# Kernel tuning notes

Measured on AMD Instinct MI355X. Metric: run time of the kernel, lower is better.

## Reference

```python
import jax, jax.numpy as jnp
import numpy as np

NUM_HEADS = 4
WINDOW = 64  # 8*8


def setup_inputs() -> dict:
    key = jax.random.key(0)
    ks = jax.random.split(key, 8)
    C = 128
    x = jax.random.normal(ks[0], (16, C, 128, 128), dtype=jnp.float32)
    s = 0.02
    Wq = jax.random.normal(ks[1], (C, C), dtype=jnp.float32) * s
    bq = jax.random.normal(ks[2], (C,), dtype=jnp.float32) * s
    Wk = jax.random.normal(ks[3], (C, C), dtype=jnp.float32) * s
    bk = jax.random.normal(ks[4], (C,), dtype=jnp.float32) * s
    Wv = jax.random.normal(ks[5], (C, C), dtype=jnp.float32) * s
    bv = jax.random.normal(ks[6], (C,), dtype=jnp.float32) * s
    Bbias = jnp.zeros((WINDOW, WINDOW), dtype=jnp.float32)
    return {"x": x, "Wq": Wq, "bq": bq, "Wk": Wk, "bk": bk, "Wv": Wv, "bv": bv, "Bbias": Bbias}


def reference(x, Wq, bq, Wk, bk, Wv, bv, Bbias):
    B, C, H, W = x.shape
    nW = (H * W) // WINDOW
    h = NUM_HEADS
    d = C // h
    # (B,C,H,W) -> (B,H,W,C) -> (B, nW, WINDOW, C)
    xr = jnp.transpose(x, (0, 2, 3, 1)).reshape(B, nW, WINDOW, C)
    # torch Linear: y = x @ W.T + b
    q = xr @ Wq.T + bq
    k = xr @ Wk.T + bk
    v = xr @ Wv.T + bv
    # split heads: (B, nW, WINDOW, h, d) -> (B, nW, h, WINDOW, d)
    def split(t):
        return jnp.transpose(t.reshape(B, nW, WINDOW, h, d), (0, 1, 3, 2, 4))
    Q, K, V = split(q), split(k), split(v)
    scale = 1.0 / jnp.sqrt(jnp.asarray(d, dtype=x.dtype))
    scores = jnp.einsum('bnhqd,bnhkd->bnhqk', Q, K) * scale + Bbias
    probs = jax.nn.softmax(scores, axis=-1)
    out = jnp.einsum('bnhqk,bnhkd->bnhqd', probs, V)
    # (B, nW, h, WINDOW, d) -> (B, nW, WINDOW, C) -> (B,H,W,C) -> (B,C,H,W)
    out = jnp.transpose(out, (0, 1, 3, 2, 4)).reshape(B, H, W, C)
    return jnp.transpose(out, (0, 3, 1, 2))
```

## Files before the change

kernel.cpp:

```cpp
#include <hip/hip_runtime.h>
#include <hip/hip_bf16.h>


typedef __attribute__((ext_vector_type(8))) short bf16x8;
typedef __attribute__((ext_vector_type(4))) float f32x4;

__device__ __forceinline__ ushort f2bf(float f) {
    __hip_bfloat16 h = __float2bfloat16(f);
    ushort u; __builtin_memcpy(&u, &h, 2); return u;
}
__device__ __forceinline__ unsigned pk2(float a, float b) {
    __hip_bfloat162 h = __float22bfloat162_rn(make_float2(a, b));
    unsigned u; __builtin_memcpy(&u, &h, 4); return u;
}
__device__ __forceinline__ int fsw(int row) { return ((row ^ (row >> 4)) & 15) << 4; }

__global__ void wconv(const float* __restrict__ Wq, const float* __restrict__ Wk,
                      const float* __restrict__ Wv, ushort* __restrict__ out) {
    int i = blockIdx.x * 256 + threadIdx.x;
    out[i]         = f2bf(Wq[i]);
    out[16384 + i] = f2bf(Wk[i]);
    out[32768 + i] = f2bf(Wv[i]);
}

__global__ __launch_bounds__(256, 2)
void attn_win(const float* __restrict__ x, const ushort* __restrict__ wbf,
              const float* __restrict__ bq, const float* __restrict__ bk,
              const float* __restrict__ bv, const float* __restrict__ Bb,
              float* __restrict__ out) {
    __shared__ __align__(16) char sX[16384];

    const int tid = threadIdx.x;
    const int w = tid >> 6;
    const int l = tid & 63;
    const int lr = l & 15;
    const int lg = (l >> 4) & 3;
    const int blk = blockIdx.x;
    const int b = blk >> 8, n = blk & 255;
    const long xbase = (long)b * 128 * 16384 + n * 64;

    const int s0 = 32 * (lg & 1) + lr;
    const int s1 = s0 + 16;
    const bool hi2 = (lg >> 1);

    #pragma unroll
    for (int it = 0; it < 2; ++it) {
        int idx = it * 256 + tid;
        int cq = idx >> 4, t4 = idx & 15;
        const float* px = x + xbase + (long)(4 * cq) * 16384 + t4 * 4;
        float4 v0 = *(const float4*)(px);
        float4 v1 = *(const float4*)(px + 16384);
        float4 v2 = *(const float4*)(px + 32768);
        float4 v3 = *(const float4*)(px + 49152);
        float a0[4] = {v0.x, v0.y, v0.z, v0.w};
        float a1[4] = {v1.x, v1.y, v1.z, v1.w};
        float a2[4] = {v2.x, v2.y, v2.z, v2.w};
        float a3[4] = {v3.x, v3.y, v3.z, v3.w};
        #pragma unroll
        for (int jj = 0; jj < 4; ++jj) {
            int t = t4 * 4 + jj;
            uint2 pk;
            pk.x = pk2(a0[jj], a1[jj]);
            pk.y = pk2(a2[jj], a3[jj]);
            *(uint2*)(sX + t * 256 + ((8 * cq) ^ fsw(t))) = pk;
        }
    }
    __syncthreads();

    bf16x8 fQ[4], fK[4];
    {
        f32x4 accQ[2][4], accK[2][4];
        #pragma unroll
        for (int tn = 0; tn < 2; ++tn) {
            float4 bbq = *(const float4*)(bq + 32 * w + 16 * tn + 4 * lg);
            float4 bbk = *(const float4*)(bk + 32 * w + 16 * tn + 4 * lg);
            #pragma unroll
            for (int tm = 0; tm < 4; ++tm) {
                accQ[tn][tm] = (f32x4){bbq.x, bbq.y, bbq.z, bbq.w};
                accK[tn][tm] = (f32x4){bbk.x, bbk.y, bbk.z, bbk.w};
            }
        }
        #pragma unroll
        for (int kk = 0; kk < 4; ++kk) {
            bf16x8 aXk[4];
            #pragma unroll
            for (int tm = 0; tm < 4; ++tm) {
                int row = 16 * tm + lr;
                aXk[tm] = *(const bf16x8*)(sX + row * 256
                              + (((8 * lg + 32 * kk) * 2) ^ fsw(row)));
            }
            bf16x8 bWq[2], bWk[2];
            #pragma unroll
            for (int tn = 0; tn < 2; ++tn) {
                int orow = (32 * w + 16 * tn + lr) * 128 + 8 * lg + 32 * kk;
                bWq[tn] = *(const bf16x8*)(wbf + orow);
                bWk[tn] = *(const bf16x8*)(wbf + 16384 + orow);
            }
            #pragma unroll
            for (int tn = 0; tn < 2; ++tn)
                #pragma unroll
                for (int tm = 0; tm < 4; ++tm) {
                    accQ[tn][tm] = __builtin_amdgcn_mfma_f32_16x16x32_bf16(
                        bWq[tn], aXk[tm], accQ[tn][tm], 0, 0, 0);
                    accK[tn][tm] = __builtin_amdgcn_mfma_f32_16x16x32_bf16(
                        bWk[tn], aXk[tm], accK[tn][tm], 0, 0, 0);
                }
        }
        #pragma unroll
        for (int p = 0; p < 2; ++p) {
            unsigned qpk[4][2][2];
            #pragma unroll
            for (int tm = 0; tm < 4; ++tm)
                #pragma unroll
                for (int tn = 0; tn < 2; ++tn) {
                    const f32x4& a = (p == 0) ? accQ[tn][tm] : accK[tn][tm];
                    qpk[tm][tn][0] = pk2(a[0], a[1]);
                    qpk[tm][tn][1] = pk2(a[2], a[3]);
                }
            #pragma unroll
            for (int tm = 0; tm < 4; ++tm) {
                int t00 = __shfl((int)qpk[tm][0][0], s0);
                int t01 = __shfl((int)qpk[tm][0][1], s0);
                int t10 = __shfl((int)qpk[tm][1][0], s0);
                int t11 = __shfl((int)qpk[tm][1][1], s0);
                int u00 = __shfl((int)qpk[tm][0][0], s1);
                int u01 = __shfl((int)qpk[tm][0][1], s1);
                int u10 = __shfl((int)qpk[tm][1][0], s1);
                int u11 = __shfl((int)qpk[tm][1][1], s1);
                int4 wv;
                wv.x = hi2 ? t10 : t00;
                wv.y = hi2 ? t11 : t01;
                wv.z = hi2 ? u10 : u00;
                wv.w = hi2 ? u11 : u01;
                if (p == 0) fQ[tm] = *(bf16x8*)&wv;
                else        fK[tm] = *(bf16x8*)&wv;
            }
        }
    }

    bf16x8 fV[2][2];
    {
        const ushort* wp = wbf + 32768;
        f32x4 acc[4][2];
        #pragma unroll
        for (int tn = 0; tn < 2; ++tn) {
            float bias = bv[32 * w + 16 * tn + lr];
            #pragma unroll
            for (int tmi = 0; tmi < 4; ++tmi)
                acc[tmi][tn] = (f32x4){bias, bias, bias, bias};
        }
        #pragma unroll
        for (int kk = 0; kk < 4; ++kk) {
            bf16x8 aXk[4];
            #pragma unroll
            for (int tmi = 0; tmi < 4; ++tmi) {
                int row = 16 * tmi + lr;
                aXk[tmi] = *(const bf16x8*)(sX + row * 256
                               + (((8 * lg + 32 * kk) * 2) ^ fsw(row)));
            }
            bf16x8 bW[2];
            #pragma unroll
            for (int tn = 0; tn < 2; ++tn)
                bW[tn] = *(const bf16x8*)(wp + (32 * w + 16 * tn + lr) * 128 + 8 * lg + 32 * kk);
            #pragma unroll
            for (int tmi = 0; tmi < 4; ++tmi)
                #pragma unroll
                for (int tn = 0; tn < 2; ++tn)
                    acc[tmi][tn] = __builtin_amdgcn_mfma_f32_16x16x32_bf16(
                        aXk[tmi], bW[tn], acc[tmi][tn], 0, 0, 0);
        }
        unsigned vpk[4][2][2];
        #pragma unroll
        for (int tmi = 0; tmi < 4; ++tmi)
            #pragma unroll
            for (int tn = 0; tn < 2; ++tn) {
                vpk[tmi][tn][0] = pk2(acc[tmi][tn][0], acc[tmi][tn][1]);
                vpk[tmi][tn][1] = pk2(acc[tmi][tn][2], acc[tmi][tn][3]);
            }
        #pragma unroll
        for (int kk2 = 0; kk2 < 2; ++kk2)
            #pragma unroll
            for (int tn = 0; tn < 2; ++tn) {
                int tmA = 2 * kk2, tmB = 2 * kk2 + 1;
                int a0 = __shfl((int)vpk[tmA][tn][0], s0);
                int a1 = __shfl((int)vpk[tmA][tn][1], s0);
                int a2 = __shfl((int)vpk[tmA][tn][0], s1);
                int a3 = __shfl((int)vpk[tmA][tn][1], s1);
                int b0 = __shfl((int)vpk[tmB][tn][0], s0);
                int b1 = __shfl((int)vpk[tmB][tn][1], s0);
                int b2 = __shfl((int)vpk[tmB][tn][0], s1);
                int b3 = __shfl((int)vpk[tmB][tn][1], s1);
                int4 wv;
                wv.x = hi2 ? b0 : a0;
                wv.y = hi2 ? b1 : a1;
                wv.z = hi2 ? b2 : a2;
                wv.w = hi2 ? b3 : a3;
                fV[kk2][tn] = *(bf16x8*)&wv;
            }
    }

    f32x4 sc[4][4];
    #pragma unroll
    for (int tmK = 0; tmK < 4; ++tmK)
        #pragma unroll
        for (int tmQ = 0; tmQ < 4; ++tmQ) {
            sc[tmK][tmQ] = (f32x4){0.f, 0.f, 0.f, 0.f};
            sc[tmK][tmQ] = __builtin_amdgcn_mfma_f32_16x16x32_bf16(
                fK[tmK], fQ[tmQ], sc[tmK][tmQ], 0, 0, 0);
        }

    const float scale = 0.17677669529663687f;
    const float L2E = 1.4426950408889634f;
    #pragma unroll
    for (int tmQ = 0; tmQ < 4; ++tmQ) {
        int q = 16 * tmQ + lr;
        float s = 0.f;
        #pragma unroll
        for (int tmK = 0; tmK < 4; ++tmK) {
            float4 bb = *(const float4*)(Bb + q * 64 + 16 * tmK + 4 * lg);
            float e0 = exp2f((sc[tmK][tmQ][0] * scale + bb.x) * L2E);
            float e1 = exp2f((sc[tmK][tmQ][1] * scale + bb.y) * L2E);
            float e2 = exp2f((sc[tmK][tmQ][2] * scale + bb.z) * L2E);
            float e3 = exp2f((sc[tmK][tmQ][3] * scale + bb.w) * L2E);
            sc[tmK][tmQ][0] = e0; sc[tmK][tmQ][1] = e1;
            sc[tmK][tmQ][2] = e2; sc[tmK][tmQ][3] = e3;
            s += (e0 + e1) + (e2 + e3);
        }
        s += __shfl_xor(s, 16);
        s += __shfl_xor(s, 32);
        float rs = 1.0f / s;
        #pragma unroll
        for (int tmK = 0; tmK < 4; ++tmK)
            #pragma unroll
            for (int r = 0; r < 4; ++r)
                sc[tmK][tmQ][r] *= rs;
    }

    unsigned pks[4][4][2];
    #pragma unroll
    for (int tmK = 0; tmK < 4; ++tmK)
        #pragma unroll
        for (int tmQ = 0; tmQ < 4; ++tmQ) {
            pks[tmK][tmQ][0] = pk2(sc[tmK][tmQ][0], sc[tmK][tmQ][1]);
            pks[tmK][tmQ][1] = pk2(sc[tmK][tmQ][2], sc[tmK][tmQ][3]);
        }

    f32x4 o[4][2];
    #pragma unroll
    for (int tmq = 0; tmq < 4; ++tmq)
        #pragma unroll
        for (int tn = 0; tn < 2; ++tn)
            o[tmq][tn] = (f32x4){0.f, 0.f, 0.f, 0.f};
    #pragma unroll
    for (int kk2 = 0; kk2 < 2; ++kk2) {
        int tmA = 2 * kk2, tmB = 2 * kk2 + 1;
        #pragma unroll
        for (int tmq = 0; tmq < 4; ++tmq) {
            int a0 = __shfl((int)pks[tmA][tmq][0], s0);
            int b0 = __shfl((int)pks[tmB][tmq][0], s0);
            int a1 = __shfl((int)pks[tmA][tmq][1], s0);
            int b1 = __shfl((int)pks[tmB][tmq][1], s0);
            int a2 = __shfl((int)pks[tmA][tmq][0], s1);
            int b2 = __shfl((int)pks[tmB][tmq][0], s1);
            int a3 = __shfl((int)pks[tmA][tmq][1], s1);
            int b3 = __shfl((int)pks[tmB][tmq][1], s1);
            int4 wv;
            wv.x = hi2 ? b0 : a0;
            wv.y = hi2 ? b1 : a1;
            wv.z = hi2 ? b2 : a2;
            wv.w = hi2 ? b3 : a3;
            bf16x8 aP = *(bf16x8*)&wv;
            #pragma unroll
            for (int tn = 0; tn < 2; ++tn)
                o[tmq][tn] = __builtin_amdgcn_mfma_f32_16x16x32_bf16(
                    aP, fV[kk2][tn], o[tmq][tn], 0, 0, 0);
        }
    }

    #pragma unroll
    for (int tmq = 0; tmq < 4; ++tmq)
        #pragma unroll
        for (int tn = 0; tn < 2; ++tn) {
            int ch = 32 * w + 16 * tn + lr;
            int tok = 16 * tmq + 4 * lg;
            float4 ov;
            ov.x = o[tmq][tn][0];
            ov.y = o[tmq][tn][1];
            ov.z = o[tmq][tn][2];
            ov.w = o[tmq][tn][3];
            *(float4*)(out + xbase + (long)ch * 16384 + tok) = ov;
        }
}

extern "C" void kernel_launch(void* const* d_in, const int* in_sizes, int n_in,
                              void* d_out, int out_size, void* d_ws, size_t ws_size,
                              hipStream_t stream) {
    const float* x  = (const float*)d_in[0];
    const float* Wq = (const float*)d_in[1];
    const float* bq = (const float*)d_in[2];
    const float* Wk = (const float*)d_in[3];
    const float* bk = (const float*)d_in[4];
    const float* Wv = (const float*)d_in[5];
    const float* bv = (const float*)d_in[6];
    const float* Bb = (const float*)d_in[7];
    float* out = (float*)d_out;
    ushort* wbf = (ushort*)d_ws;

    wconv<<<64, 256, 0, stream>>>(Wq, Wk, Wv, wbf);
    attn_win<<<4096, 256, 0, stream>>>(x, wbf, bq, bk, bv, Bb, out);
}
```

Measured before the change: 114.3 us.

## Process two windows per block with all global loads issued up front

Each block now handles two adjacent 64-token windows, so the grid is halved. Every x load for both windows is issued before any conversion, which puts more memory requests in flight per thread. The two windows are then computed one after another from separate LDS buffers. Shared memory doubles to 32KB and register pressure during the load phase rises, which may cut occupancy. Compute for the second window does not overlap with loads for a later block.

After: 199.8 us. 1.75x slower.

```diff
diff --git a/kernel.cpp b/kernel.cpp
--- a/kernel.cpp
+++ b/kernel.cpp
@@ -28,7 +28,7 @@
               const float* __restrict__ bq, const float* __restrict__ bk,
               const float* __restrict__ bv, const float* __restrict__ Bb,
               float* __restrict__ out) {
-    __shared__ __align__(16) char sX[16384];
+    __shared__ __align__(16) char sX[2][16384];
 
     const int tid = threadIdx.x;
     const int w = tid >> 6;
@@ -36,260 +36,278 @@
     const int lr = l & 15;
     const int lg = (l >> 4) & 3;
     const int blk = blockIdx.x;
-    const int b = blk >> 8, n = blk & 255;
-    const long xbase = (long)b * 128 * 16384 + n * 64;
+    const int gw0 = 2 * blk;
+    const long xbase0 = (long)(gw0 >> 8) * 128 * 16384 + (long)(gw0 & 255) * 64;
 
     const int s0 = 32 * (lg & 1) + lr;
     const int s1 = s0 + 16;
     const bool hi2 = (lg >> 1);
 
-    #pragma unroll
-    for (int it = 0; it < 2; ++it) {
-        int idx = it * 256 + tid;
-        int cq = idx >> 4, t4 = idx & 15;
-        const float* px = x + xbase + (long)(4 * cq) * 16384 + t4 * 4;
-        float4 v0 = *(const float4*)(px);
-        float4 v1 = *(const float4*)(px + 16384);
-        float4 v2 = *(const float4*)(px + 32768);
-        float4 v3 = *(const float4*)(px + 49152);
-        float a0[4] = {v0.x, v0.y, v0.z, v0.w};
-        float a1[4] = {v1.x, v1.y, v1.z, v1.w};
-        float a2[4] = {v2.x, v2.y, v2.z, v2.w};
-        float a3[4] = {v3.x, v3.y, v3.z, v3.w};
-        #pragma unroll
-        for (int jj = 0; jj < 4; ++jj) {
-            int t = t4 * 4 + jj;
-            uint2 pk;
-            pk.x = pk2(a0[jj], a1[jj]);
-            pk.y = pk2(a2[jj], a3[jj]);
-            *(uint2*)(sX + t * 256 + ((8 * cq) ^ fsw(t))) = pk;
-        }
+    {
+        float4 pf[2][2][4];
+        #pragma unroll
+        for (int wi = 0; wi < 2; ++wi)
+            #pragma unroll
+            for (int it = 0; it < 2; ++it) {
+                int idx = it * 256 + tid;
+                int cq = idx >> 4, t4 = idx & 15;
+                const float* px = x + xbase0 + wi * 64 + (long)(4 * cq) * 16384 + t4 * 4;
+                pf[wi][it][0] = *(const float4*)(px);
+                pf[wi][it][1] = *(const float4*)(px + 16384);
+                pf[wi][it][2] = *(const float4*)(px + 32768);
+                pf[wi][it][3] = *(const float4*)(px + 49152);
+            }
+        #pragma unroll
+        for (int wi = 0; wi < 2; ++wi)
+            #pragma unroll
+            for (int it = 0; it < 2; ++it) {
+                int idx = it * 256 + tid;
+                int cq = idx >> 4, t4 = idx & 15;
+                float a0[4] = {pf[wi][it][0].x, pf[wi][it][0].y, pf[wi][it][0].z, pf[wi][it][0].w};
+                float a1[4] = {pf[wi][it][1].x, pf[wi][it][1].y, pf[wi][it][1].z, pf[wi][it][1].w};
+                float a2[4] = {pf[wi][it][2].x, pf[wi][it][2].y, pf[wi][it][2].z, pf[wi][it][2].w};
+                float a3[4] = {pf[wi][it][3].x, pf[wi][it][3].y, pf[wi][it][3].z, pf[wi][it][3].w};
+                #pragma unroll
+                for (int jj = 0; jj < 4; ++jj) {
+                    int t = t4 * 4 + jj;
+                    uint2 pk;
+                    pk.x = pk2(a0[jj], a1[jj]);
+                    pk.y = pk2(a2[jj], a3[jj]);
+                    *(uint2*)(&sX[wi][0] + t * 256 + ((8 * cq) ^ fsw(t))) = pk;
+                }
+            }
     }
     __syncthreads();
 
-    bf16x8 fQ[4], fK[4];
-    {
-        f32x4 accQ[2][4], accK[2][4];
-        #pragma unroll
-        for (int tn = 0; tn < 2; ++tn) {
-            float4 bbq = *(const float4*)(bq + 32 * w + 16 * tn + 4 * lg);
-            float4 bbk = *(const float4*)(bk + 32 * w + 16 * tn + 4 * lg);
-            #pragma unroll
-            for (int tm = 0; tm < 4; ++tm) {
-                accQ[tn][tm] = (f32x4){bbq.x, bbq.y, bbq.z, bbq.w};
-                accK[tn][tm] = (f32x4){bbk.x, bbk.y, bbk.z, bbk.w};
+    #pragma unroll 1
+    for (int wi = 0; wi < 2; ++wi) {
+        const char* sXw = &sX[wi][0];
+        const long xb = xbase0 + wi * 64;
+
+        bf16x8 fQ[4], fK[4];
+        {
+            f32x4 accQ[2][4], accK[2][4];
+            #pragma unroll
+            for (int tn = 0; tn < 2; ++tn) {
+                float4 bbq = *(const float4*)(bq + 32 * w + 16 * tn + 4 * lg);
+                float4 bbk = *(const float4*)(bk + 32 * w + 16 * tn + 4 * lg);
+                #pragma unroll
+                for (int tm = 0; tm < 4; ++tm) {
+                    accQ[tn][tm] = (f32x4){bbq.x, bbq.y, bbq.z, bbq.w};
+                    accK[tn][tm] = (f32x4){bbk.x, bbk.y, bbk.z, bbk.w};
+                }
+            }
+            #pragma unroll
+            for (int kk = 0; kk < 4; ++kk) {
+                bf16x8 aXk[4];
+                #pragma unroll
+                for (int tm = 0; tm < 4; ++tm) {
+                    int row = 16 * tm + lr;
+                    aXk[tm] = *(const bf16x8*)(sXw + row * 256
+                                  + (((8 * lg + 32 * kk) * 2) ^ fsw(row)));
+                }
+                bf16x8 bWq[2], bWk[2];
+                #pragma unroll
+                for (int tn = 0; tn < 2; ++tn) {
+                    int orow = (32 * w + 16 * tn + lr) * 128 + 8 * lg + 32 * kk;
+                    bWq[tn] = *(const bf16x8*)(wbf + orow);
+                    bWk[tn] = *(const bf16x8*)(wbf + 16384 + orow);
+                }
+                #pragma unroll
+                for (int tn = 0; tn < 2; ++tn)
+                    #pragma unroll
+                    for (int tm = 0; tm < 4; ++tm) {
+                        accQ[tn][tm] = __builtin_amdgcn_mfma_f32_16x16x32_bf16(
+                            bWq[tn], aXk[tm], accQ[tn][tm], 0, 0, 0);
+                        accK[tn][tm] = __builtin_amdgcn_mfma_f32_16x16x32_bf16(
+                            bWk[tn], aXk[tm], accK[tn][tm], 0, 0, 0);
+                    }
+            }
+            #pragma unroll
+            for (int p = 0; p < 2; ++p) {
+                unsigned qpk[4][2][2];
+                #pragma unroll
+                for (int tm = 0; tm < 4; ++tm)
+                    #pragma unroll
+                    for (int tn = 0; tn < 2; ++tn) {
+                        const f32x4& a = (p == 0) ? accQ[tn][tm] : accK[tn][tm];
+                        qpk[tm][tn][0] = pk2(a[0], a[1]);
+                        qpk[tm][tn][1] = pk2(a[2], a[3]);
+                    }
+                #pragma unroll
+                for (int tm = 0; tm < 4; ++tm) {
+                    int t00 = __shfl((int)qpk[tm][0][0], s0);
+                    int t01 = __shfl((int)qpk[tm][0][1], s0);
+                    int t10 = __shfl((int)qpk[tm][1][0], s0);
+                    int t11 = __shfl((int)qpk[tm][1][1], s0);
+                    int u00 = __shfl((int)qpk[tm][0][0], s1);
+                    int u01 = __shfl((int)qpk[tm][0][1], s1);
+                    int u10 = __shfl((int)qpk[tm][1][0], s1);
+                    int u11 = __shfl((int)qpk[tm][1][1], s1);
+                    int4 wv;
+                    wv.x = hi2 ? t10 : t00;
+                    wv.y = hi2 ? t11 : t01;
+                    wv.z = hi2 ? u10 : u00;
+                    wv.w = hi2 ? u11 : u01;
+                    if (p == 0) fQ[tm] = *(bf16x8*)&wv;
+                    else        fK[tm] = *(bf16x8*)&wv;
+                }
             }
         }
-        #pragma unroll
-        for (int kk = 0; kk < 4; ++kk) {
-            bf16x8 aXk[4];
-            #pragma unroll
-            for (int tm = 0; tm < 4; ++tm) {
-                int row = 16 * tm + lr;
-                aXk[tm] = *(const bf16x8*)(sX + row * 256
-                              + (((8 * lg + 32 * kk) * 2) ^ fsw(row)));
-            }
-            bf16x8 bWq[2], bWk[2];
+
+        bf16x8 fV[2][2];
+        {
+            const ushort* wp = wbf + 32768;
+            f32x4 acc[4][2];
             #pragma unroll
             for (int tn = 0; tn < 2; ++tn) {
-                int orow = (32 * w + 16 * tn + lr) * 128 + 8 * lg + 32 * kk;
-                bWq[tn] = *(const bf16x8*)(wbf + orow);
-                bWk[tn] = *(const bf16x8*)(wbf + 16384 + orow);
-            }
+                float bias = bv[32 * w + 16 * tn + lr];
+                #pragma unroll
+                for (int tmi = 0; tmi < 4; ++tmi)
+                    acc[tmi][tn] = (f32x4){bias, bias, bias, bias};
+            }
+            #pragma unroll
+            for (int kk = 0; kk < 4; ++kk) {
+                bf16x8 aXk[4];
+                #pragma unroll
+                for (int tmi = 0; tmi < 4; ++tmi) {
+                    int row = 16 * tmi + lr;
+                    aXk[tmi] = *(const bf16x8*)(sXw + row * 256
+                                   + (((8 * lg + 32 * kk) * 2) ^ fsw(row)));
+                }
+                bf16x8 bW[2];
+                #pragma unroll
+                for (int tn = 0; tn < 2; ++tn)
+                    bW[tn] = *(const bf16x8*)(wp + (32 * w + 16 * tn + lr) * 128 + 8 * lg + 32 * kk);
+                #pragma unroll
+                for (int tmi = 0; tmi < 4; ++tmi)
+                    #pragma unroll
+                    for (int tn = 0; tn < 2; ++tn)
+                        acc[tmi][tn] = __builtin_amdgcn_mfma_f32_16x16x32_bf16(
+                            aXk[tmi], bW[tn], acc[tmi][tn], 0, 0, 0);
+            }
+            unsigned vpk[4][2][2];
+            #pragma unroll
+            for (int tmi = 0; tmi < 4; ++tmi)
+                #pragma unroll
+                for (int tn = 0; tn < 2; ++tn) {
+                    vpk[tmi][tn][0] = pk2(acc[tmi][tn][0], acc[tmi][tn][1]);
+                    vpk[tmi][tn][1] = pk2(acc[tmi][tn][2], acc[tmi][tn][3]);
+                }
+            #pragma unroll
+            for (int kk2 = 0; kk2 < 2; ++kk2)
+                #pragma unroll
+                for (int tn = 0; tn < 2; ++tn) {
+                    int tmA = 2 * kk2, tmB = 2 * kk2 + 1;
+                    int a0 = __shfl((int)vpk[tmA][tn][0], s0);
+                    int a1 = __shfl((int)vpk[tmA][tn][1], s0);
+                    int a2 = __shfl((int)vpk[tmA][tn][0], s1);
+                    int a3 = __shfl((int)vpk[tmA][tn][1], s1);
+                    int b0 = __shfl((int)vpk[tmB][tn][0], s0);
+                    int b1 = __shfl((int)vpk[tmB][tn][1], s0);
+                    int b2 = __shfl((int)vpk[tmB][tn][0], s1);
+                    int b3 = __shfl((int)vpk[tmB][tn][1], s1);
+                    int4 wv;
+                    wv.x = hi2 ? b0 : a0;
+                    wv.y = hi2 ? b1 : a1;
+                    wv.z = hi2 ? b2 : a2;
+                    wv.w = hi2 ? b3 : a3;
+                    fV[kk2][tn] = *(bf16x8*)&wv;
+                }
+        }
+
+        f32x4 sc[4][4];
+        #pragma unroll
+        for (int tmK = 0; tmK < 4; ++tmK)
+            #pragma unroll
+            for (int tmQ = 0; tmQ < 4; ++tmQ) {
+                sc[tmK][tmQ] = (f32x4){0.f, 0.f, 0.f, 0.f};
+                sc[tmK][tmQ] = __builtin_amdgcn_mfma_f32_16x16x32_bf16(
+                    fK[tmK], fQ[tmQ], sc[tmK][tmQ], 0, 0, 0);
+            }
+
+        const float scale = 0.17677669529663687f;
+        const float L2E = 1.4426950408889634f;
+        #pragma unroll
+        for (int tmQ = 0; tmQ < 4; ++tmQ) {
+            int q = 16 * tmQ + lr;
+            float s = 0.f;
+            #pragma unroll
+            for (int tmK = 0; tmK < 4; ++tmK) {
+                float4 bb = *(const float4*)(Bb + q * 64 + 16 * tmK + 4 * lg);
+                float e0 = exp2f((sc[tmK][tmQ][0] * scale + bb.x) * L2E);
+                float e1 = exp2f((sc[tmK][tmQ][1] * scale + bb.y) * L2E);
+                float e2 = exp2f((sc[tmK][tmQ][2] * scale + bb.z) * L2E);
+                float e3 = exp2f((sc[tmK][tmQ][3] * scale + bb.w) * L2E);
+                sc[tmK][tmQ][0] = e0; sc[tmK][tmQ][1] = e1;
+                sc[tmK][tmQ][2] = e2; sc[tmK][tmQ][3] = e3;
+                s += (e0 + e1) + (e2 + e3);
+            }
+            s += __shfl_xor(s, 16);
+            s += __shfl_xor(s, 32);
+            float rs = 1.0f / s;
+            #pragma unroll
+            for (int tmK = 0; tmK < 4; ++tmK)
+                #pragma unroll
+                for (int r = 0; r < 4; ++r)
+                    sc[tmK][tmQ][r] *= rs;
+        }
+
+        unsigned pks[4][4][2];
+        #pragma unroll
+        for (int tmK = 0; tmK < 4; ++tmK)
+            #pragma unroll
+            for (int tmQ = 0; tmQ < 4; ++tmQ) {
+                pks[tmK][tmQ][0] = pk2(sc[tmK][tmQ][0], sc[tmK][tmQ][1]);
+                pks[tmK][tmQ][1] = pk2(sc[tmK][tmQ][2], sc[tmK][tmQ][3]);
+            }
+
+        f32x4 o[4][2];
+        #pragma unroll
+        for (int tmq = 0; tmq < 4; ++tmq)
             #pragma unroll
             for (int tn = 0; tn < 2; ++tn)
-                #pragma unroll
-                for (int tm = 0; tm < 4; ++tm) {
-                    accQ[tn][tm] = __builtin_amdgcn_mfma_f32_16x16x32_bf16(
-                        bWq[tn], aXk[tm], accQ[tn][tm], 0, 0, 0);
-                    accK[tn][tm] = __builtin_amdgcn_mfma_f32_16x16x32_bf16(
-                        bWk[tn], aXk[tm], accK[tn][tm], 0, 0, 0);
-                }
-        }
-        #pragma unroll
-        for (int p = 0; p < 2; ++p) {
-            unsigned qpk[4][2][2];
-            #pragma unroll
-            for (int tm = 0; tm < 4; ++tm)
-                #pragma unroll
-                for (int tn = 0; tn < 2; ++tn) {
-                    const f32x4& a = (p == 0) ? accQ[tn][tm] : accK[tn][tm];
-                    qpk[tm][tn][0] = pk2(a[0], a[1]);
-                    qpk[tm][tn][1] = pk2(a[2], a[3]);
-                }
-            #pragma unroll
-            for (int tm = 0; tm < 4; ++tm) {
-                int t00 = __shfl((int)qpk[tm][0][0], s0);
-                int t01 = __shfl((int)qpk[tm][0][1], s0);
-                int t10 = __shfl((int)qpk[tm][1][0], s0);
-                int t11 = __shfl((int)qpk[tm][1][1], s0);
-                int u00 = __shfl((int)qpk[tm][0][0], s1);
-                int u01 = __shfl((int)qpk[tm][0][1], s1);
-                int u10 = __shfl((int)qpk[tm][1][0], s1);
-                int u11 = __shfl((int)qpk[tm][1][1], s1);
-                int4 wv;
-                wv.x = hi2 ? t10 : t00;
-                wv.y = hi2 ? t11 : t01;
-                wv.z = hi2 ? u10 : u00;
-                wv.w = hi2 ? u11 : u01;
-                if (p == 0) fQ[tm] = *(bf16x8*)&wv;
-                else        fK[tm] = *(bf16x8*)&wv;
-            }
-        }
-    }
-
-    bf16x8 fV[2][2];
-    {
-        const ushort* wp = wbf + 32768;
-        f32x4 acc[4][2];
-        #pragma unroll
-        for (int tn = 0; tn < 2; ++tn) {
-            float bias = bv[32 * w + 16 * tn + lr];
-            #pragma unroll
-            for (int tmi = 0; tmi < 4; ++tmi)
-                acc[tmi][tn] = (f32x4){bias, bias, bias, bias};
-        }
-        #pragma unroll
-        for (int kk = 0; kk < 4; ++kk) {
-            bf16x8 aXk[4];
-            #pragma unroll
-            for (int tmi = 0; tmi < 4; ++tmi) {
-                int row = 16 * tmi + lr;
-                aXk[tmi] = *(const bf16x8*)(sX + row * 256
-                               + (((8 * lg + 32 * kk) * 2) ^ fsw(row)));
-            }
-            bf16x8 bW[2];
-            #pragma unroll
-            for (int tn = 0; tn < 2; ++tn)
-                bW[tn] = *(const bf16x8*)(wp + (32 * w + 16 * tn + lr) * 128 + 8 * lg + 32 * kk);
-            #pragma unroll
-            for (int tmi = 0; tmi < 4; ++tmi)
-                #pragma unroll
-                for (int tn = 0; tn < 2; ++tn)
-                    acc[tmi][tn] = __builtin_amdgcn_mfma_f32_16x16x32_bf16(
-                        aXk[tmi], bW[tn], acc[tmi][tn], 0, 0, 0);
-        }
-        unsigned vpk[4][2][2];
-        #pragma unroll
-        for (int tmi = 0; tmi < 4; ++tmi)
-            #pragma unroll
-            for (int tn = 0; tn < 2; ++tn) {
-                vpk[tmi][tn][0] = pk2(acc[tmi][tn][0], acc[tmi][tn][1]);
-                vpk[tmi][tn][1] = pk2(acc[tmi][tn][2], acc[tmi][tn][3]);
-            }
-        #pragma unroll
-        for (int kk2 = 0; kk2 < 2; ++kk2)
-            #pragma unroll
-            for (int tn = 0; tn < 2; ++tn) {
-                int tmA = 2 * kk2, tmB = 2 * kk2 + 1;
-                int a0 = __shfl((int)vpk[tmA][tn][0], s0);
-                int a1 = __shfl((int)vpk[tmA][tn][1], s0);
-                int a2 = __shfl((int)vpk[tmA][tn][0], s1);
-                int a3 = __shfl((int)vpk[tmA][tn][1], s1);
-                int b0 = __shfl((int)vpk[tmB][tn][0], s0);
-                int b1 = __shfl((int)vpk[tmB][tn][1], s0);
-                int b2 = __shfl((int)vpk[tmB][tn][0], s1);
-                int b3 = __shfl((int)vpk[tmB][tn][1], s1);
+                o[tmq][tn] = (f32x4){0.f, 0.f, 0.f, 0.f};
+        #pragma unroll
+        for (int kk2 = 0; kk2 < 2; ++kk2) {
+            int tmA = 2 * kk2, tmB = 2 * kk2 + 1;
+            #pragma unroll
+            for (int tmq = 0; tmq < 4; ++tmq) {
+                int a0 = __shfl((int)pks[tmA][tmq][0], s0);
+                int b0 = __shfl((int)pks[tmB][tmq][0], s0);
+                int a1 = __shfl((int)pks[tmA][tmq][1], s0);
+                int b1 = __shfl((int)pks[tmB][tmq][1], s0);
+                int a2 = __shfl((int)pks[tmA][tmq][0], s1);
+                int b2 = __shfl((int)pks[tmB][tmq][0], s1);
+                int a3 = __shfl((int)pks[tmA][tmq][1], s1);
+                int b3 = __shfl((int)pks[tmB][tmq][1], s1);
                 int4 wv;
                 wv.x = hi2 ? b0 : a0;
                 wv.y = hi2 ? b1 : a1;
                 wv.z = hi2 ? b2 : a2;
                 wv.w = hi2 ? b3 : a3;
-                fV[kk2][tn] = *(bf16x8*)&wv;
+                bf16x8 aP = *(bf16x8*)&wv;
+                #pragma unroll
+                for (int tn = 0; tn < 2; ++tn)
+                    o[tmq][tn] = __builtin_amdgcn_mfma_f32_16x16x32_bf16(
+                        aP, fV[kk2][tn], o[tmq][tn], 0, 0, 0);
+            }
+        }
+
+        #pragma unroll
+        for (int tmq = 0; tmq < 4; ++tmq)
+            #pragma unroll
+            for (int tn = 0; tn < 2; ++tn) {
+                int ch = 32 * w + 16 * tn + lr;
+                int tok = 16 * tmq + 4 * lg;
+                float4 ov;
+                ov.x = o[tmq][tn][0];
+                ov.y = o[tmq][tn][1];
+                ov.z = o[tmq][tn][2];
+                ov.w = o[tmq][tn][3];
+                *(float4*)(out + xb + (long)ch * 16384 + tok) = ov;
             }
     }
-
-    f32x4 sc[4][4];
-    #pragma unroll
-    for (int tmK = 0; tmK < 4; ++tmK)
-        #pragma unroll
-        for (int tmQ = 0; tmQ < 4; ++tmQ) {
-            sc[tmK][tmQ] = (f32x4){0.f, 0.f, 0.f, 0.f};
-            sc[tmK][tmQ] = __builtin_amdgcn_mfma_f32_16x16x32_bf16(
-                fK[tmK], fQ[tmQ], sc[tmK][tmQ], 0, 0, 0);
-        }
-
-    const float scale = 0.17677669529663687f;
-    const float L2E = 1.4426950408889634f;
-    #pragma unroll
-    for (int tmQ = 0; tmQ < 4; ++tmQ) {
-        int q = 16 * tmQ + lr;
-        float s = 0.f;
-        #pragma unroll
-        for (int tmK = 0; tmK < 4; ++tmK) {
-            float4 bb = *(const float4*)(Bb + q * 64 + 16 * tmK + 4 * lg);
-            float e0 = exp2f((sc[tmK][tmQ][0] * scale + bb.x) * L2E);
-            float e1 = exp2f((sc[tmK][tmQ][1] * scale + bb.y) * L2E);
-            float e2 = exp2f((sc[tmK][tmQ][2] * scale + bb.z) * L2E);
-            float e3 = exp2f((sc[tmK][tmQ][3] * scale + bb.w) * L2E);
-            sc[tmK][tmQ][0] = e0; sc[tmK][tmQ][1] = e1;
-            sc[tmK][tmQ][2] = e2; sc[tmK][tmQ][3] = e3;
-            s += (e0 + e1) + (e2 + e3);
-        }
-        s += __shfl_xor(s, 16);
-        s += __shfl_xor(s, 32);
-        float rs = 1.0f / s;
-        #pragma unroll
-        for (int tmK = 0; tmK < 4; ++tmK)
-            #pragma unroll
-            for (int r = 0; r < 4; ++r)
-                sc[tmK][tmQ][r] *= rs;
-    }
-
-    unsigned pks[4][4][2];
-    #pragma unroll
-    for (int tmK = 0; tmK < 4; ++tmK)
-        #pragma unroll
-        for (int tmQ = 0; tmQ < 4; ++tmQ) {
-            pks[tmK][tmQ][0] = pk2(sc[tmK][tmQ][0], sc[tmK][tmQ][1]);
-            pks[tmK][tmQ][1] = pk2(sc[tmK][tmQ][2], sc[tmK][tmQ][3]);
-        }
-
-    f32x4 o[4][2];
-    #pragma unroll
-    for (int tmq = 0; tmq < 4; ++tmq)
-        #pragma unroll
-        for (int tn = 0; tn < 2; ++tn)
-            o[tmq][tn] = (f32x4){0.f, 0.f, 0.f, 0.f};
-    #pragma unroll
-    for (int kk2 = 0; kk2 < 2; ++kk2) {
-        int tmA = 2 * kk2, tmB = 2 * kk2 + 1;
-        #pragma unroll
-        for (int tmq = 0; tmq < 4; ++tmq) {
-            int a0 = __shfl((int)pks[tmA][tmq][0], s0);
-            int b0 = __shfl((int)pks[tmB][tmq][0], s0);
-            int a1 = __shfl((int)pks[tmA][tmq][1], s0);
-            int b1 = __shfl((int)pks[tmB][tmq][1], s0);
-            int a2 = __shfl((int)pks[tmA][tmq][0], s1);
-            int b2 = __shfl((int)pks[tmB][tmq][0], s1);
-            int a3 = __shfl((int)pks[tmA][tmq][1], s1);
-            int b3 = __shfl((int)pks[tmB][tmq][1], s1);
-            int4 wv;
-            wv.x = hi2 ? b0 : a0;
-            wv.y = hi2 ? b1 : a1;
-            wv.z = hi2 ? b2 : a2;
-            wv.w = hi2 ? b3 : a3;
-            bf16x8 aP = *(bf16x8*)&wv;
-            #pragma unroll
-            for (int tn = 0; tn < 2; ++tn)
-                o[tmq][tn] = __builtin_amdgcn_mfma_f32_16x16x32_bf16(
-                    aP, fV[kk2][tn], o[tmq][tn], 0, 0, 0);
-        }
-    }
-
-    #pragma unroll
-    for (int tmq = 0; tmq < 4; ++tmq)
-        #pragma unroll
-        for (int tn = 0; tn < 2; ++tn) {
-            int ch = 32 * w + 16 * tn + lr;
-            int tok = 16 * tmq + 4 * lg;
-            float4 ov;
-            ov.x = o[tmq][tn][0];
-            ov.y = o[tmq][tn][1];
-            ov.z = o[tmq][tn][2];
-            ov.w = o[tmq][tn][3];
-            *(float4*)(out + xbase + (long)ch * 16384 + tok) = ov;
-        }
 }
 
 extern "C" void kernel_launch(void* const* d_in, const int* in_sizes, int n_in,
@@ -307,5 +325,5 @@
     ushort* wbf = (ushort*)d_ws;
 
     wconv<<<64, 256, 0, stream>>>(Wq, Wk, Wv, wbf);
-    attn_win<<<4096, 256, 0, stream>>>(x, wbf, bq, bk, bv, Bb, out);
-}
+    attn_win<<<2048, 256, 0, stream>>>(x, wbf, bq, bk, bv, Bb, out);
+}
```

## Switch to 16x16x16 bf16 MFMA so accumulators feed next GEMM without shuffles

Applied to the files above, without the earlier changes.

Replaces the 16x16x32 bf16 MFMA with the 16x16x16 variant throughout the QKV projection, QK^T and PV stages. With K=16, the accumulator layout of one MFMA matches the operand layout the next one needs, so the cross-lane __shfl permutations that rebuilt Q, K, V and P fragments are dropped and results are packed to bf16 in place. The cost is twice as many MFMA instructions, each covering half the K depth, plus narrower 8-byte LDS and global loads. Score computation is also moved inside the per-query-tile softmax loop, which shortens register live ranges.

New measurement: 162.5 us. +42.2%, slower.

```diff
diff --git a/kernel.cpp b/kernel.cpp
--- a/kernel.cpp
+++ b/kernel.cpp
@@ -2,8 +2,10 @@
 #include <hip/hip_bf16.h>
 
 
-typedef __attribute__((ext_vector_type(8))) short bf16x8;
+typedef __attribute__((ext_vector_type(4))) short bf16x4;
 typedef __attribute__((ext_vector_type(4))) float f32x4;
+
+#define MFMA16(A, B, C) __builtin_amdgcn_mfma_f32_16x16x16bf16_1k((A), (B), (C), 0, 0, 0)
 
 __device__ __forceinline__ ushort f2bf(float f) {
     __hip_bfloat16 h = __float2bfloat16(f);
@@ -12,6 +14,10 @@
 __device__ __forceinline__ unsigned pk2(float a, float b) {
     __hip_bfloat162 h = __float22bfloat162_rn(make_float2(a, b));
     unsigned u; __builtin_memcpy(&u, &h, 4); return u;
+}
+__device__ __forceinline__ bf16x4 pk4(float a, float b, float c, float d) {
+    uint2 u; u.x = pk2(a, b); u.y = pk2(c, d);
+    bf16x4 r; __builtin_memcpy(&r, &u, 8); return r;
 }
 __device__ __forceinline__ int fsw(int row) { return ((row ^ (row >> 4)) & 15) << 4; }
 
@@ -38,10 +44,6 @@
     const int blk = blockIdx.x;
     const int b = blk >> 8, n = blk & 255;
     const long xbase = (long)b * 128 * 16384 + n * 64;
-
-    const int s0 = 32 * (lg & 1) + lr;
-    const int s1 = s0 + 16;
-    const bool hi2 = (lg >> 1);
 
     #pragma unroll
     for (int it = 0; it < 2; ++it) {
@@ -67,163 +69,113 @@
     }
     __syncthreads();
 
-    bf16x8 fQ[4], fK[4];
-    {
-        f32x4 accQ[2][4], accK[2][4];
-        #pragma unroll
-        for (int tn = 0; tn < 2; ++tn) {
-            float4 bbq = *(const float4*)(bq + 32 * w + 16 * tn + 4 * lg);
-            float4 bbk = *(const float4*)(bk + 32 * w + 16 * tn + 4 * lg);
+    f32x4 accQ[2][4], accK[2][4];
+    #pragma unroll
+    for (int tn = 0; tn < 2; ++tn) {
+        float4 bbq = *(const float4*)(bq + 32 * w + 16 * tn + 4 * lg);
+        float4 bbk = *(const float4*)(bk + 32 * w + 16 * tn + 4 * lg);
+        #pragma unroll
+        for (int tm = 0; tm < 4; ++tm) {
+            accQ[tn][tm] = (f32x4){bbq.x, bbq.y, bbq.z, bbq.w};
+            accK[tn][tm] = (f32x4){bbk.x, bbk.y, bbk.z, bbk.w};
+        }
+    }
+    #pragma unroll
+    for (int kk = 0; kk < 8; ++kk) {
+        bf16x4 aXk[4];
+        #pragma unroll
+        for (int tm = 0; tm < 4; ++tm) {
+            int row = 16 * tm + lr;
+            aXk[tm] = *(const bf16x4*)(sX + row * 256
+                          + ((32 * kk + 8 * lg) ^ fsw(row)));
+        }
+        bf16x4 wq[2], wk[2];
+        #pragma unroll
+        for (int tn = 0; tn < 2; ++tn) {
+            int off = (32 * w + 16 * tn + lr) * 128 + 16 * kk + 4 * lg;
+            wq[tn] = *(const bf16x4*)(wbf + off);
+            wk[tn] = *(const bf16x4*)(wbf + 16384 + off);
+        }
+        #pragma unroll
+        for (int tn = 0; tn < 2; ++tn)
             #pragma unroll
             for (int tm = 0; tm < 4; ++tm) {
-                accQ[tn][tm] = (f32x4){bbq.x, bbq.y, bbq.z, bbq.w};
-                accK[tn][tm] = (f32x4){bbk.x, bbk.y, bbk.z, bbk.w};
+                accQ[tn][tm] = MFMA16(wq[tn], aXk[tm], accQ[tn][tm]);
+                accK[tn][tm] = MFMA16(wk[tn], aXk[tm], accK[tn][tm]);
             }
-        }
-        #pragma unroll
-        for (int kk = 0; kk < 4; ++kk) {
-            bf16x8 aXk[4];
-            #pragma unroll
-            for (int tm = 0; tm < 4; ++tm) {
-                int row = 16 * tm + lr;
-                aXk[tm] = *(const bf16x8*)(sX + row * 256
-                              + (((8 * lg + 32 * kk) * 2) ^ fsw(row)));
-            }
-            bf16x8 bWq[2], bWk[2];
-            #pragma unroll
-            for (int tn = 0; tn < 2; ++tn) {
-                int orow = (32 * w + 16 * tn + lr) * 128 + 8 * lg + 32 * kk;
-                bWq[tn] = *(const bf16x8*)(wbf + orow);
-                bWk[tn] = *(const bf16x8*)(wbf + 16384 + orow);
-            }
-            #pragma unroll
-            for (int tn = 0; tn < 2; ++tn)
-                #pragma unroll
-                for (int tm = 0; tm < 4; ++tm) {
-                    accQ[tn][tm] = __builtin_amdgcn_mfma_f32_16x16x32_bf16(
-                        bWq[tn], aXk[tm], accQ[tn][tm], 0, 0, 0);
-                    accK[tn][tm] = __builtin_amdgcn_mfma_f32_16x16x32_bf16(
-                        bWk[tn], aXk[tm], accK[tn][tm], 0, 0, 0);
-                }
-        }
-        #pragma unroll
-        for (int p = 0; p < 2; ++p) {
-            unsigned qpk[4][2][2];
-            #pragma unroll
-            for (int tm = 0; tm < 4; ++tm)
-                #pragma unroll
-                for (int tn = 0; tn < 2; ++tn) {
-                    const f32x4& a = (p == 0) ? accQ[tn][tm] : accK[tn][tm];
-                    qpk[tm][tn][0] = pk2(a[0], a[1]);
-                    qpk[tm][tn][1] = pk2(a[2], a[3]);
-                }
-            #pragma unroll
-            for (int tm = 0; tm < 4; ++tm) {
-                int t00 = __shfl((int)qpk[tm][0][0], s0);
-                int t01 = __shfl((int)qpk[tm][0][1], s0);
-                int t10 = __shfl((int)qpk[tm][1][0], s0);
-                int t11 = __shfl((int)qpk[tm][1][1], s0);
-                int u00 = __shfl((int)qpk[tm][0][0], s1);
-                int u01 = __shfl((int)qpk[tm][0][1], s1);
-                int u10 = __shfl((int)qpk[tm][1][0], s1);
-                int u11 = __shfl((int)qpk[tm][1][1], s1);
-                int4 wv;
-                wv.x = hi2 ? t10 : t00;
-                wv.y = hi2 ? t11 : t01;
-                wv.z = hi2 ? u10 : u00;
-                wv.w = hi2 ? u11 : u01;
-                if (p == 0) fQ[tm] = *(bf16x8*)&wv;
-                else        fK[tm] = *(bf16x8*)&wv;
-            }
-        }
-    }
-
-    bf16x8 fV[2][2];
+    }
+    bf16x4 fQ[4][2], fK[4][2];
+    #pragma unroll
+    for (int tm = 0; tm < 4; ++tm)
+        #pragma unroll
+        for (int tn = 0; tn < 2; ++tn) {
+            fQ[tm][tn] = pk4(accQ[tn][tm][0], accQ[tn][tm][1],
+                             accQ[tn][tm][2], accQ[tn][tm][3]);
+            fK[tm][tn] = pk4(accK[tn][tm][0], accK[tn][tm][1],
+                             accK[tn][tm][2], accK[tn][tm][3]);
+        }
+
+    bf16x4 fV[4][2];
     {
         const ushort* wp = wbf + 32768;
-        f32x4 acc[4][2];
+        f32x4 accV[4][2];
         #pragma unroll
         for (int tn = 0; tn < 2; ++tn) {
             float bias = bv[32 * w + 16 * tn + lr];
             #pragma unroll
             for (int tmi = 0; tmi < 4; ++tmi)
-                acc[tmi][tn] = (f32x4){bias, bias, bias, bias};
-        }
-        #pragma unroll
-        for (int kk = 0; kk < 4; ++kk) {
-            bf16x8 aXk[4];
+                accV[tmi][tn] = (f32x4){bias, bias, bias, bias};
+        }
+        #pragma unroll
+        for (int kk = 0; kk < 8; ++kk) {
+            bf16x4 aXk[4];
             #pragma unroll
             for (int tmi = 0; tmi < 4; ++tmi) {
                 int row = 16 * tmi + lr;
-                aXk[tmi] = *(const bf16x8*)(sX + row * 256
-                               + (((8 * lg + 32 * kk) * 2) ^ fsw(row)));
+                aXk[tmi] = *(const bf16x4*)(sX + row * 256
+                               + ((32 * kk + 8 * lg) ^ fsw(row)));
             }
-            bf16x8 bW[2];
+            bf16x4 wv[2];
             #pragma unroll
             for (int tn = 0; tn < 2; ++tn)
-                bW[tn] = *(const bf16x8*)(wp + (32 * w + 16 * tn + lr) * 128 + 8 * lg + 32 * kk);
+                wv[tn] = *(const bf16x4*)(wp + (32 * w + 16 * tn + lr) * 128 + 16 * kk + 4 * lg);
             #pragma unroll
             for (int tmi = 0; tmi < 4; ++tmi)
                 #pragma unroll
                 for (int tn = 0; tn < 2; ++tn)
-                    acc[tmi][tn] = __builtin_amdgcn_mfma_f32_16x16x32_bf16(
-                        aXk[tmi], bW[tn], acc[tmi][tn], 0, 0, 0);
-        }
-        unsigned vpk[4][2][2];
+                    accV[tmi][tn] = MFMA16(aXk[tmi], wv[tn], accV[tmi][tn]);
+        }
         #pragma unroll
         for (int tmi = 0; tmi < 4; ++tmi)
             #pragma unroll
-            for (int tn = 0; tn < 2; ++tn) {
-                vpk[tmi][tn][0] = pk2(acc[tmi][tn][0], acc[tmi][tn][1]);
-                vpk[tmi][tn][1] = pk2(acc[tmi][tn][2], acc[tmi][tn][3]);
-            }
-        #pragma unroll
-        for (int kk2 = 0; kk2 < 2; ++kk2)
-            #pragma unroll
-            for (int tn = 0; tn < 2; ++tn) {
-                int tmA = 2 * kk2, tmB = 2 * kk2 + 1;
-                int a0 = __shfl((int)vpk[tmA][tn][0], s0);
-                int a1 = __shfl((int)vpk[tmA][tn][1], s0);
-                int a2 = __shfl((int)vpk[tmA][tn][0], s1);
-                int a3 = __shfl((int)vpk[tmA][tn][1], s1);
-                int b0 = __shfl((int)vpk[tmB][tn][0], s0);
-                int b1 = __shfl((int)vpk[tmB][tn][1], s0);
-                int b2 = __shfl((int)vpk[tmB][tn][0], s1);
-                int b3 = __shfl((int)vpk[tmB][tn][1], s1);
-                int4 wv;
-                wv.x = hi2 ? b0 : a0;
-                wv.y = hi2 ? b1 : a1;
-                wv.z = hi2 ? b2 : a2;
-                wv.w = hi2 ? b3 : a3;
-                fV[kk2][tn] = *(bf16x8*)&wv;
-            }
-    }
-
-    f32x4 sc[4][4];
-    #pragma unroll
-    for (int tmK = 0; tmK < 4; ++tmK)
-        #pragma unroll
-        for (int tmQ = 0; tmQ < 4; ++tmQ) {
-            sc[tmK][tmQ] = (f32x4){0.f, 0.f, 0.f, 0.f};
-            sc[tmK][tmQ] = __builtin_amdgcn_mfma_f32_16x16x32_bf16(
-                fK[tmK], fQ[tmQ], sc[tmK][tmQ], 0, 0, 0);
-        }
+            for (int tn = 0; tn < 2; ++tn)
+                fV[tmi][tn] = pk4(accV[tmi][tn][0], accV[tmi][tn][1],
+                                  accV[tmi][tn][2], accV[tmi][tn][3]);
+    }
 
     const float scale = 0.17677669529663687f;
     const float L2E = 1.4426950408889634f;
+    bf16x4 pP[4][4];
     #pragma unroll
     for (int tmQ = 0; tmQ < 4; ++tmQ) {
+        f32x4 sc[4];
+        #pragma unroll
+        for (int tmK = 0; tmK < 4; ++tmK) {
+            sc[tmK] = (f32x4){0.f, 0.f, 0.f, 0.f};
+            sc[tmK] = MFMA16(fK[tmK][0], fQ[tmQ][0], sc[tmK]);
+            sc[tmK] = MFMA16(fK[tmK][1], fQ[tmQ][1], sc[tmK]);
+        }
         int q = 16 * tmQ + lr;
         float s = 0.f;
         #pragma unroll
         for (int tmK = 0; tmK < 4; ++tmK) {
             float4 bb = *(const float4*)(Bb + q * 64 + 16 * tmK + 4 * lg);
-            float e0 = exp2f((sc[tmK][tmQ][0] * scale + bb.x) * L2E);
-            float e1 = exp2f((sc[tmK][tmQ][1] * scale + bb.y) * L2E);
-            float e2 = exp2f((sc[tmK][tmQ][2] * scale + bb.z) * L2E);
-            float e3 = exp2f((sc[tmK][tmQ][3] * scale + bb.w) * L2E);
-            sc[tmK][tmQ][0] = e0; sc[tmK][tmQ][1] = e1;
-            sc[tmK][tmQ][2] = e2; sc[tmK][tmQ][3] = e3;
+            float e0 = exp2f((sc[tmK][0] * scale + bb.x) * L2E);
+            float e1 = exp2f((sc[tmK][1] * scale + bb.y) * L2E);
+            float e2 = exp2f((sc[tmK][2] * scale + bb.z) * L2E);
+            float e3 = exp2f((sc[tmK][3] * scale + bb.w) * L2E);
+            sc[tmK][0] = e0; sc[tmK][1] = e1;
+            sc[tmK][2] = e2; sc[tmK][3] = e3;
             s += (e0 + e1) + (e2 + e3);
         }
         s += __shfl_xor(s, 16);
@@ -231,19 +183,9 @@
         float rs = 1.0f / s;
         #pragma unroll
         for (int tmK = 0; tmK < 4; ++tmK)
-            #pragma unroll
-            for (int r = 0; r < 4; ++r)
-                sc[tmK][tmQ][r] *= rs;
-    }
-
-    unsigned pks[4][4][2];
-    #pragma unroll
-    for (int tmK = 0; tmK < 4; ++tmK)
-        #pragma unroll
-        for (int tmQ = 0; tmQ < 4; ++tmQ) {
-            pks[tmK][tmQ][0] = pk2(sc[tmK][tmQ][0], sc[tmK][tmQ][1]);
-            pks[tmK][tmQ][1] = pk2(sc[tmK][tmQ][2], sc[tmK][tmQ][3]);
-        }
+            pP[tmK][tmQ] = pk4(sc[tmK][0] * rs, sc[tmK][1] * rs,
+                               sc[tmK][2] * rs, sc[tmK][3] * rs);
+    }
 
     f32x4 o[4][2];
     #pragma unroll
@@ -252,30 +194,12 @@
         for (int tn = 0; tn < 2; ++tn)
             o[tmq][tn] = (f32x4){0.f, 0.f, 0.f, 0.f};
     #pragma unroll
-    for (int kk2 = 0; kk2 < 2; ++kk2) {
-        int tmA = 2 * kk2, tmB = 2 * kk2 + 1;
-        #pragma unroll
-        for (int tmq = 0; tmq < 4; ++tmq) {
-            int a0 = __shfl((int)pks[tmA][tmq][0], s0);
-            int b0 = __shfl((int)pks[tmB][tmq][0], s0);
-            int a1 = __shfl((int)pks[tmA][tmq][1], s0);
-            int b1 = __shfl((int)pks[tmB][tmq][1], s0);
-            int a2 = __shfl((int)pks[tmA][tmq][0], s1);
-            int b2 = __shfl((int)pks[tmB][tmq][0], s1);
-            int a3 = __shfl((int)pks[tmA][tmq][1], s1);
-            int b3 = __shfl((int)pks[tmB][tmq][1], s1);
-            int4 wv;
-            wv.x = hi2 ? b0 : a0;
-            wv.y = hi2 ? b1 : a1;
-            wv.z = hi2 ? b2 : a2;
-            wv.w = hi2 ? b3 : a3;
-            bf16x8 aP = *(bf16x8*)&wv;
+    for (int tmK = 0; tmK < 4; ++tmK)
+        #pragma unroll
+        for (int tmq = 0; tmq < 4; ++tmq)
             #pragma unroll
             for (int tn = 0; tn < 2; ++tn)
-                o[tmq][tn] = __builtin_amdgcn_mfma_f32_16x16x32_bf16(
-                    aP, fV[kk2][tn], o[tmq][tn], 0, 0, 0);
-        }
-    }
+                o[tmq][tn] = MFMA16(pP[tmK][tmq], fV[tmK][tn], o[tmq][tn]);
 
     #pragma unroll
     for (int tmq = 0; tmq < 4; ++tmq)
```
